# Performance work log

Measured on AMD Instinct MI355X. Metric: run time of the kernel, lower is better.

## Reference

```python
import math
import jax, jax.numpy as jnp
import numpy as np

# ---- config (from ModelConfig) ----
HIDDEN = 2880
HEAD_DIM = 64
N_HEADS = 64
N_KV = 8
Q_MULT = N_HEADS // N_KV  # 8
SLIDING_WINDOW = 128      # left context; causal windowed attention
ROPE_BASE = 150000.0
ROPE_SCALE = 32.0
NTK_ALPHA = 1.0
NTK_BETA = 32.0
INIT_CTX = 4096
RMS_EPS = 1e-5
SM_SCALE = 1.0 / math.sqrt(HEAD_DIM)
Q_DIM = N_HEADS * HEAD_DIM   # 4096
KV_DIM = N_KV * HEAD_DIM     # 512
QKV_DIM = Q_DIM + 2 * KV_DIM # 5120
B, T = 1, 2048


def _rope_cos_sin(n_tokens):
    """YaRN-scaled rotary cache, per RotaryEmbedding._compute_concentration_and_inv_freq."""
    d_half = HEAD_DIM // 2
    freq = ROPE_BASE ** (jnp.arange(0, HEAD_DIM, 2, dtype=jnp.float32) / HEAD_DIM)
    concentration = 0.1 * math.log(ROPE_SCALE) + 1.0
    low = d_half * math.log(INIT_CTX / (NTK_BETA * 2 * math.pi)) / math.log(ROPE_BASE)
    high = d_half * math.log(INIT_CTX / (NTK_ALPHA * 2 * math.pi)) / math.log(ROPE_BASE)
    interpolation = 1.0 / (ROPE_SCALE * freq)
    extrapolation = 1.0 / freq
    ramp = (jnp.arange(d_half, dtype=jnp.float32) - low) / (high - low)
    mask = 1.0 - jnp.clip(ramp, 0.0, 1.0)
    inv_freq = interpolation * (1.0 - mask) + extrapolation * mask
    pos = jnp.arange(n_tokens, dtype=jnp.float32)
    angles = pos[:, None] * inv_freq[None, :]  # [t, d/2]
    return jnp.cos(angles) * concentration, jnp.sin(angles) * concentration


def _apply_rope(x, cos, sin):
    """Interleaved RoPE (matches _apply_rotary_emb). x: [b, t, ..., d]."""
    shape = x.shape
    n_mid = x.ndim - 3  # dims between token axis and feature axis
    c = cos.reshape((1, shape[1]) + (1,) * n_mid + (shape[-1] // 2,))
    s = sin.reshape((1, shape[1]) + (1,) * n_mid + (shape[-1] // 2,))
    x1 = x[..., ::2]
    x2 = x[..., 1::2]
    o1 = x1 * c - x2 * s
    o2 = x2 * c + x1 * s
    return jnp.stack((o1, o2), axis=-1).reshape(shape)


def _rmsnorm(x, scale):
    t = x.astype(jnp.float32)
    t = t * jax.lax.rsqrt(jnp.mean(t * t, axis=-1, keepdims=True) + RMS_EPS)
    return (t * scale).astype(x.dtype)


def setup_inputs() -> dict:
    key = jax.random.key(0)
    ks = jax.random.split(key, 7)
    x = jax.random.normal(ks[0], (B, T, HIDDEN), dtype=jnp.float32)
    norm_scale = jnp.ones((HIDDEN,), dtype=jnp.float32)
    w_qkv = jax.random.normal(ks[1], (QKV_DIM, HIDDEN), dtype=jnp.float32) * (HIDDEN ** -0.5)
    b_qkv = jax.random.normal(ks[2], (QKV_DIM,), dtype=jnp.float32) * 0.02
    sinks = jax.random.normal(ks[3], (N_HEADS,), dtype=jnp.float32)
    w_out = jax.random.normal(ks[4], (HIDDEN, Q_DIM), dtype=jnp.float32) * (Q_DIM ** -0.5)
    b_out = jax.random.normal(ks[5], (HIDDEN,), dtype=jnp.float32) * 0.02
    return {"x": x, "norm_scale": norm_scale, "w_qkv": w_qkv, "b_qkv": b_qkv,
            "sinks": sinks, "w_out": w_out, "b_out": b_out}


def reference(x, norm_scale, w_qkv, b_qkv, sinks, w_out, b_out):
    b, t, _ = x.shape
    h = _rmsnorm(x, norm_scale)
    qkv = h @ w_qkv.T + b_qkv  # [b, t, 5120]
    q = qkv[..., :Q_DIM].reshape(b, t, N_KV, Q_MULT, HEAD_DIM)
    k = qkv[..., Q_DIM:Q_DIM + KV_DIM].reshape(b, t, N_KV, HEAD_DIM)
    v = qkv[..., Q_DIM + KV_DIM:].reshape(b, t, N_KV, HEAD_DIM)

    cos, sin = _rope_cos_sin(t)
    q = _apply_rope(q, cos, sin)
    k = _apply_rope(k, cos, sin)

    # sliding-window causal attention with sink logits (sdpa windowed path)
    left_ctx = SLIDING_WINDOW
    window = left_ctx + 1
    kp = jnp.pad(k, ((0, 0), (left_ctx, 0), (0, 0), (0, 0)))
    vp = jnp.pad(v, ((0, 0), (left_ctx, 0), (0, 0), (0, 0)))
    gather_idx = jnp.arange(t)[:, None] + jnp.arange(window)[None, :]  # into padded axis
    kwin = kp[:, gather_idx]  # [b, t, w, n_kv, d]
    vwin = vp[:, gather_idx]

    pos = jnp.arange(t)[:, None] + (jnp.arange(window) - left_ctx)[None, :]
    valid = (pos >= 0) & (pos < t)  # [t, w]

    scores = jnp.einsum('bthqd,btwhd->bthqw', q, kwin).astype(jnp.float32) * SM_SCALE
    scores = jnp.where(valid[None, :, None, None, :], scores, -jnp.inf)

    sink = (sinks * math.log(2.0)).reshape(N_KV, Q_MULT)
    sink = jnp.broadcast_to(sink[None, None, :, :, None], (b, t, N_KV, Q_MULT, 1))
    scores = jnp.concatenate([scores, sink], axis=-1)  # [b, t, h, q, w+1]

    w_attn = jax.nn.softmax(scores, axis=-1)[..., :-1].astype(v.dtype)
    attn = jnp.einsum('bthqw,btwhd->bthqd', w_attn, vwin).reshape(b, t, -1)

    out = attn @ w_out.T + b_out
    return x + out
```

## Files before the change

kernel.cpp:

```cpp
#include <hip/hip_runtime.h>
#include <math.h>

typedef unsigned short u16;
typedef unsigned int   u32;
using f32x4  = __attribute__((ext_vector_type(4))) float;
using bf16x8 = __attribute__((ext_vector_type(8))) __bf16;

#define HIDDEN   2880
#define QKVD     5120
#define QD       4096
#define TTOK     2048
#define NKV      8
#define QMULT    8
#define HD       64
#define NPAD     2944

#define PREP_QKV_BLOCKS  14400
#define PREP_WOUT_BLOCKS 11776
#define PREP_RMS_BLOCKS  2048

static __device__ __forceinline__ float bflo(u32 u){ return __uint_as_float(u << 16); }
static __device__ __forceinline__ float bfhi(u32 u){ return __uint_as_float(u & 0xffff0000u); }
static __device__ __forceinline__ u16 f2bf(float f){
    u32 u = __float_as_uint(f);
    u32 r = (u + 0x7fffu + ((u >> 16) & 1u)) >> 16;
    return (u16)r;
}

static __device__ __forceinline__ void glds16(const void* g, void* l) {
    __builtin_amdgcn_global_load_lds(
        (__attribute__((address_space(1))) void*)g,
        (__attribute__((address_space(3))) void*)l,
        16, 0, 0);
}

__global__ __launch_bounds__(256) void prep_kernel(const float* __restrict__ w_qkv,
                                                   u16* __restrict__ wqkv_bf,
                                                   const float* __restrict__ w_out,
                                                   u16* __restrict__ wout_bf,
                                                   const float* __restrict__ x,
                                                   const float* __restrict__ scale,
                                                   u16* __restrict__ h) {
    const int b = blockIdx.x;
    const int tid = threadIdx.x;
    if (b < PREP_QKV_BLOCKS) {
        int i = b * 256 + tid;
        float4 f = ((const float4*)w_qkv)[i];
        ushort4 o;
        o.x = f2bf(f.x); o.y = f2bf(f.y); o.z = f2bf(f.z); o.w = f2bf(f.w);
        ((ushort4*)wqkv_bf)[i] = o;
    } else if (b < PREP_QKV_BLOCKS + PREP_WOUT_BLOCKS) {
        int i = (b - PREP_QKV_BLOCKS) * 256 + tid;
        int idx = i * 4;
        int row = idx >> 12;
        int col = idx & 4095;
        ushort4 o;
        if (row < HIDDEN) {
            float4 f = *(const float4*)(w_out + (long)row * QD + col);
            o.x = f2bf(f.x); o.y = f2bf(f.y); o.z = f2bf(f.z); o.w = f2bf(f.w);
        } else {
            o.x = 0; o.y = 0; o.z = 0; o.w = 0;
        }
        ((ushort4*)wout_bf)[i] = o;
    } else {
        const int t = b - (PREP_QKV_BLOCKS + PREP_WOUT_BLOCKS);
        const float4* xr = (const float4*)(x + (long)t * HIDDEN);
        float4 v[3];
        float ss = 0.f;
        #pragma unroll
        for (int it = 0; it < 3; ++it) {
            int i4 = tid + it * 256;
            if (i4 < 720) {
                v[it] = xr[i4];
                ss += v[it].x*v[it].x + v[it].y*v[it].y + v[it].z*v[it].z + v[it].w*v[it].w;
            }
        }
        #pragma unroll
        for (int off = 32; off > 0; off >>= 1) ss += __shfl_down(ss, off);
        __shared__ float red[4];
        if ((tid & 63) == 0) red[tid >> 6] = ss;
        __syncthreads();
        float tot = red[0] + red[1] + red[2] + red[3];
        float rr = rsqrtf(tot * (1.0f / HIDDEN) + 1e-5f);
        ushort4* hr = (ushort4*)(h + (long)t * HIDDEN);
        #pragma unroll
        for (int it = 0; it < 3; ++it) {
            int i4 = tid + it * 256;
            if (i4 < 720) {
                float4 s4 = ((const float4*)scale)[i4];
                ushort4 o;
                o.x = f2bf(v[it].x * rr * s4.x);
                o.y = f2bf(v[it].y * rr * s4.y);
                o.z = f2bf(v[it].z * rr * s4.z);
                o.w = f2bf(v[it].w * rr * s4.w);
                hr[i4] = o;
            }
        }
    }
}

__global__ __launch_bounds__(256) void gemm_bt_part(const u16* __restrict__ A,
                                                    const u16* __restrict__ B,
                                                    u16* __restrict__ C0,
                                                    int N, int K, int ksplit) {
    __shared__ u16 lsA[2][128 * 32];
    __shared__ u16 lsB[2][128 * 32];
    const int tid  = threadIdx.x;
    const int lane = tid & 63;
    const int wv   = tid >> 6;
    const int wm   = wv >> 1, wn = wv & 1;
    const long m0 = (long)blockIdx.y * 128;
    const long n0 = (long)blockIdx.x * 128;
    const int kb = blockIdx.z * ksplit;
    const int ke = kb + ksplit;
    u16* C = C0 + (size_t)blockIdx.z * ((size_t)TTOK * N);

    f32x4 acc[4][4];
    #pragma unroll
    for (int i = 0; i < 4; ++i)
        #pragma unroll
        for (int j = 0; j < 4; ++j) acc[i][j] = f32x4{0.f, 0.f, 0.f, 0.f};

    const int sr = lane >> 2;
    const int sc = lane & 3;
    const int fr = lane & 15;
    const int fk = (lane >> 4) * 8;

    const u16* Abase = A + (m0 + wv * 32 + sr) * (long)K + sc * 8;
    const u16* Bbase = B + (n0 + wv * 32 + sr) * (long)K + sc * 8;
    const int ldsW = (wv * 32) * 32;
    const long rowK16 = 16 * (long)K;

    auto stage = [&](int k0, int buf) {
        glds16(Abase + k0,          &lsA[buf][ldsW]);
        glds16(Abase + k0 + rowK16, &lsA[buf][ldsW + 512]);
        glds16(Bbase + k0,          &lsB[buf][ldsW]);
        glds16(Bbase + k0 + rowK16, &lsB[buf][ldsW + 512]);
    };

    stage(kb, 0);
    int ib = 0;
    for (int k0 = kb; k0 < ke; k0 += 32, ib ^= 1) {
        __syncthreads();
        if (k0 + 32 < ke) stage(k0 + 32, ib ^ 1);
        bf16x8 af[4], bfg[4];
        #pragma unroll
        for (int mi = 0; mi < 4; ++mi)
            af[mi] = *(const bf16x8*)&lsA[ib][(wm * 64 + mi * 16 + fr) * 32 + fk];
        #pragma unroll
        for (int ni = 0; ni < 4; ++ni)
            bfg[ni] = *(const bf16x8*)&lsB[ib][(wn * 64 + ni * 16 + fr) * 32 + fk];
        #pragma unroll
        for (int mi = 0; mi < 4; ++mi)
            #pragma unroll
            for (int ni = 0; ni < 4; ++ni)
                acc[mi][ni] = __builtin_amdgcn_mfma_f32_16x16x32_bf16(af[mi], bfg[ni], acc[mi][ni], 0, 0, 0);
    }

    const int cr = (lane >> 4) * 4;
    const int cc = lane & 15;
    #pragma unroll
    for (int ni = 0; ni < 4; ++ni) {
        long col = n0 + wn * 64 + ni * 16 + cc;
        #pragma unroll
        for (int mi = 0; mi < 4; ++mi) {
            #pragma unroll
            for (int r2 = 0; r2 < 4; ++r2) {
                long row = m0 + wm * 64 + mi * 16 + cr + r2;
                C[row * (long)N + col] = f2bf(acc[mi][ni][r2]);
            }
        }
    }
}

__global__ __launch_bounds__(256) void rope_kernel(const u16* __restrict__ p1a,
                                                   const u16* __restrict__ p1b,
                                                   const float* __restrict__ b_qkv,
                                                   u16* __restrict__ qr,
                                                   u16* __restrict__ kr,
                                                   u16* __restrict__ vr) {
    const int t = blockIdx.x;
    const int tid = threadIdx.x;
    __shared__ float cs[32], sn[32];
    if (tid < 32) {
        float fi = (float)tid;
        float freq   = exp2f(17.1946032f * (fi * (1.0f / 32.0f)));
        float interp = 1.0f / (32.0f * freq);
        float extra  = 1.0f / freq;
        float ramp   = (fi - 8.0927802f) * (1.0f / (17.3980220f - 8.0927802f));
        float rc     = fminf(fmaxf(ramp, 0.0f), 1.0f);
        float invf   = interp * rc + extra * (1.0f - rc);
        float ang    = (float)t * invf;
        cs[tid] = cosf(ang) * 1.3465736f;
        sn[tid] = sinf(ang) * 1.3465736f;
    }
    __syncthreads();
    const u16* rowA = p1a + (long)t * QKVD;
    const u16* rowB = p1b + (long)t * QKVD;
    auto pair = [&](int col) -> float2 {
        u32 ua = *(const u32*)(rowA + col);
        u32 ub = *(const u32*)(rowB + col);
        float2 bb = *(const float2*)(b_qkv + col);
        return make_float2(bflo(ua) + bflo(ub) + bb.x, bfhi(ua) + bfhi(ub) + bb.y);
    };
    for (int p = tid; p < 2048; p += 256) {
        int hd2 = p >> 5, i = p & 31;
        float2 ab = pair(hd2 * 64 + 2 * i);
        float o1 = ab.x * cs[i] - ab.y * sn[i];
        float o2 = ab.y * cs[i] + ab.x * sn[i];
        *(u32*)(qr + (long)t * QD + hd2 * 64 + 2 * i) = (u32)f2bf(o1) | ((u32)f2bf(o2) << 16);
    }
    {
        int kv = tid >> 5, i = tid & 31;
        float2 ab = pair(QD + kv * 64 + 2 * i);
        float o1 = ab.x * cs[i] - ab.y * sn[i];
        float o2 = ab.y * cs[i] + ab.x * sn[i];
        *(u32*)(kr + ((long)kv * TTOK + t) * HD + 2 * i) = (u32)f2bf(o1) | ((u32)f2bf(o2) << 16);
    }
    {
        int kv = tid >> 5, d2 = tid & 31;
        float2 ab = pair(QD + 512 + kv * 64 + 2 * d2);
        *(u32*)(vr + ((long)kv * TTOK + t) * HD + 2 * d2) = (u32)f2bf(ab.x) | ((u32)f2bf(ab.y) << 16);
    }
}

__global__ __launch_bounds__(256, 2) void attn_kernel(const u16* __restrict__ qr,
                                                      const u16* __restrict__ kr,
                                                      const u16* __restrict__ vr,
                                                      const float* __restrict__ sinks,
                                                      u16* __restrict__ o) {
    const int t0  = blockIdx.x * 16;
    const int h   = blockIdx.y;
    const int qhg = blockIdx.z;
    const int tid = threadIdx.x;
    const int lane = tid & 63, wv = tid >> 6;
    __shared__ __align__(16) u16 ks[144][72];
    __shared__ __align__(16) u16 Vt[64][168];
    __shared__ __align__(16) u16 P [4][16][168];
    const u16* kb = kr + (long)h * TTOK * HD;
    const u16* vb = vr + (long)h * TTOK * HD;

    #pragma unroll
    for (int i = 0; i < 5; ++i) {
        int idx = i * 256 + tid;
        if (idx < 144 * 8) {
            int rr = idx >> 3, c = idx & 7;
            int tk = t0 - 128 + rr;
            int tks = tk < 0 ? 0 : tk;
            *(uint4*)&ks[rr][c * 8] = *(const uint4*)(kb + (long)tks * HD + c * 8);
        }
    }
    #pragma unroll
    for (int c4 = 0; c4 < 8; ++c4) {
        if (tid < 144) {
            int tk = t0 - 128 + tid;
            int tks = tk < 0 ? 0 : tk;
            uint4 v4 = *(const uint4*)(vb + (long)tks * HD + c4 * 8);
            int d0 = c4 * 8;
            Vt[d0+0][tid] = (u16)(v4.x & 0xffff); Vt[d0+1][tid] = (u16)(v4.x >> 16);
            Vt[d0+2][tid] = (u16)(v4.y & 0xffff); Vt[d0+3][tid] = (u16)(v4.y >> 16);
            Vt[d0+4][tid] = (u16)(v4.z & 0xffff); Vt[d0+5][tid] = (u16)(v4.z >> 16);
            Vt[d0+6][tid] = (u16)(v4.w & 0xffff); Vt[d0+7][tid] = (u16)(v4.w >> 16);
        }
    }
    if (tid < 128) {
        *(uint4*)&Vt[tid >> 1][144 + (tid & 1) * 8] = uint4{0, 0, 0, 0};
    }
    if (lane < 32) {
        *(uint4*)&P[wv][lane >> 1][144 + (lane & 1) * 8] = uint4{0, 0, 0, 0};
    }
    __syncthreads();

    const int qh   = qhg * 4 + wv;
    const int head = h * QMULT + qh;
    const int fr = lane & 15, fk = (lane >> 4) * 8;
    const int cr = (lane >> 4) * 4;

    const u16* qrow = qr + (long)(t0 + fr) * QD + head * HD;
    bf16x8 qf0 = *(const bf16x8*)(qrow + fk);
    bf16x8 qf1 = *(const bf16x8*)(qrow + 32 + fk);

    const int kmin = 128 - t0;
    float lsum[4] = {0.f, 0.f, 0.f, 0.f};

    for (int nt = 0; nt < 9; ++nt) {
        bf16x8 b0 = *(const bf16x8*)&ks[nt * 16 + fr][fk];
        bf16x8 b1 = *(const bf16x8*)&ks[nt * 16 + fr][32 + fk];
        f32x4 s = f32x4{0.f, 0.f, 0.f, 0.f};
        s = __builtin_amdgcn_mfma_f32_16x16x32_bf16(qf0, b0, s, 0, 0, 0);
        s = __builtin_amdgcn_mfma_f32_16x16x32_bf16(qf1, b1, s, 0, 0, 0);
        const int kk = nt * 16 + fr;
        #pragma unroll
        for (int r = 0; r < 4; ++r) {
            int row = cr + r;
            bool valid = (kk >= row) && (kk <= row + 128) && (kk >= kmin);
            float p = valid ? __expf(s[r] * 0.125f) : 0.0f;
            lsum[r] += p;
            P[wv][row][kk] = f2bf(p);
        }
    }

    f32x4 oacc[4];
    #pragma unroll
    for (int dt = 0; dt < 4; ++dt) oacc[dt] = f32x4{0.f, 0.f, 0.f, 0.f};
    #pragma unroll
    for (int k5 = 0; k5 < 5; ++k5) {
        const int k0 = k5 * 32;
        bf16x8 pa = *(const bf16x8*)&P[wv][fr][k0 + fk];
        #pragma unroll
        for (int dt = 0; dt < 4; ++dt) {
            bf16x8 vf = *(const bf16x8*)&Vt[dt * 16 + fr][k0 + fk];
            oacc[dt] = __builtin_amdgcn_mfma_f32_16x16x32_bf16(pa, vf, oacc[dt], 0, 0, 0);
        }
    }

    #pragma unroll
    for (int r = 0; r < 4; ++r) {
        float v = lsum[r];
        v += __shfl_xor(v, 1);
        v += __shfl_xor(v, 2);
        v += __shfl_xor(v, 4);
        v += __shfl_xor(v, 8);
        lsum[r] = v;
    }
    const float sk = exp2f(sinks[head]);
    float inv[4];
    #pragma unroll
    for (int r = 0; r < 4; ++r) inv[r] = 1.0f / (lsum[r] + sk);

    #pragma unroll
    for (int dt = 0; dt < 4; ++dt) {
        #pragma unroll
        for (int r = 0; r < 4; ++r) {
            o[(long)(t0 + cr + r) * QD + head * HD + dt * 16 + fr] = f2bf(oacc[dt][r] * inv[r]);
        }
    }
}

__global__ __launch_bounds__(256) void reduce2_kernel(const u16* __restrict__ p2a,
                                                      const u16* __restrict__ p2b,
                                                      const float* __restrict__ x,
                                                      const float* __restrict__ b_out,
                                                      float* __restrict__ out) {
    const int row = blockIdx.y;
    const int c4 = blockIdx.x * 256 + threadIdx.x;
    if (c4 >= 720) return;
    const int col = c4 * 4;
    ushort4 ua = *(const ushort4*)(p2a + (long)row * NPAD + col);
    ushort4 ub = *(const ushort4*)(p2b + (long)row * NPAD + col);
    float4 xv = *(const float4*)(x + (long)row * HIDDEN + col);
    float4 bv = *(const float4*)(b_out + col);
    float4 o;
    o.x = xv.x + bv.x + __uint_as_float((u32)ua.x << 16) + __uint_as_float((u32)ub.x << 16);
    o.y = xv.y + bv.y + __uint_as_float((u32)ua.y << 16) + __uint_as_float((u32)ub.y << 16);
    o.z = xv.z + bv.z + __uint_as_float((u32)ua.z << 16) + __uint_as_float((u32)ub.z << 16);
    o.w = xv.w + bv.w + __uint_as_float((u32)ua.w << 16) + __uint_as_float((u32)ub.w << 16);
    *(float4*)(out + (long)row * HIDDEN + col) = o;
}

extern "C" void kernel_launch(void* const* d_in, const int* in_sizes, int n_in,
                              void* d_out, int out_size, void* d_ws, size_t ws_size,
                              hipStream_t stream) {
    const float* x      = (const float*)d_in[0];
    const float* nscale = (const float*)d_in[1];
    const float* w_qkv  = (const float*)d_in[2];
    const float* b_qkv  = (const float*)d_in[3];
    const float* sinks  = (const float*)d_in[4];
    const float* w_out  = (const float*)d_in[5];
    const float* b_out  = (const float*)d_in[6];
    float* out = (float*)d_out;

    char* ws = (char*)d_ws;
    size_t off = 0;
    auto alloc = [&](size_t bytes) { void* p = ws + off; off += (bytes + 255) & ~(size_t)255; return p; };
    u16* wqkv_bf = (u16*)alloc((size_t)QKVD * HIDDEN * 2);
    u16* wout_bf = (u16*)alloc((size_t)NPAD * QD * 2);
    u16* h       = (u16*)alloc((size_t)TTOK * HIDDEN * 2);
    u16* p1      = (u16*)alloc((size_t)2 * TTOK * QKVD * 2);
    u16* qrot    = (u16*)alloc((size_t)TTOK * QD * 2);
    u16* krot    = (u16*)alloc((size_t)NKV * TTOK * HD * 2);
    u16* vrot    = (u16*)alloc((size_t)NKV * TTOK * HD * 2);
    u16* attn = wqkv_bf;
    u16* p2   = p1;

    prep_kernel<<<PREP_QKV_BLOCKS + PREP_WOUT_BLOCKS + PREP_RMS_BLOCKS, 256, 0, stream>>>(
        w_qkv, wqkv_bf, w_out, wout_bf, x, nscale, h);
    gemm_bt_part<<<dim3(QKVD / 128, TTOK / 128, 2), 256, 0, stream>>>(
        h, wqkv_bf, p1, QKVD, HIDDEN, HIDDEN / 2);
    rope_kernel<<<TTOK, 256, 0, stream>>>(
        p1, p1 + (size_t)TTOK * QKVD, b_qkv, qrot, krot, vrot);
    attn_kernel<<<dim3(TTOK / 16, NKV, 2), 256, 0, stream>>>(qrot, krot, vrot, sinks, attn);
    gemm_bt_part<<<dim3(NPAD / 128, TTOK / 128, 2), 256, 0, stream>>>(
        attn, wout_bf, p2, NPAD, QD, QD / 2);
    reduce2_kernel<<<dim3(3, TTOK), 256, 0, stream>>>(
        p2, p2 + (size_t)TTOK * NPAD, x, b_out, out);
}
```

Baseline: 359.4 us.

## Replace split-K GEMM with 256x256 eight-phase pipelined MFMA kernel

```diff
diff --git a/kernel.cpp b/kernel.cpp
--- a/kernel.cpp
+++ b/kernel.cpp
@@ -33,6 +33,8 @@
         (__attribute__((address_space(3))) void*)l,
         16, 0, 0);
 }
+
+#define BAR() asm volatile("s_barrier" ::: "memory")
 
 __global__ __launch_bounds__(256) void prep_kernel(const float* __restrict__ w_qkv,
                                                    u16* __restrict__ wqkv_bf,
@@ -99,62 +101,116 @@
     }
 }
 
-__global__ __launch_bounds__(256) void gemm_bt_part(const u16* __restrict__ A,
-                                                    const u16* __restrict__ B,
-                                                    u16* __restrict__ C0,
-                                                    int N, int K, int ksplit) {
-    __shared__ u16 lsA[2][128 * 32];
-    __shared__ u16 lsB[2][128 * 32];
+
+#define LOAD_AQ(MH) do { \
+    aq[0][0] = *(const bf16x8*)(aS + (2*(MH)+0)*2048 + off0); \
+    aq[0][1] = *(const bf16x8*)(aS + (2*(MH)+0)*2048 + off1); \
+    aq[1][0] = *(const bf16x8*)(aS + (2*(MH)+1)*2048 + off0); \
+    aq[1][1] = *(const bf16x8*)(aS + (2*(MH)+1)*2048 + off1); \
+} while (0)
+
+#define MFMA_Q(MH) do { \
+    __builtin_amdgcn_s_setprio(1); \
+    _Pragma("unroll") \
+    for (int i2_ = 0; i2_ < 2; ++i2_) { \
+        _Pragma("unroll") \
+        for (int ni_ = 0; ni_ < 4; ++ni_) { \
+            acc[2*(MH)+i2_][ni_] = __builtin_amdgcn_mfma_f32_16x16x32_bf16(aq[i2_][0], bq[ni_][0], acc[2*(MH)+i2_][ni_], 0, 0, 0); \
+            acc[2*(MH)+i2_][ni_] = __builtin_amdgcn_mfma_f32_16x16x32_bf16(aq[i2_][1], bq[ni_][1], acc[2*(MH)+i2_][ni_], 0, 0, 0); \
+        } \
+    } \
+    __builtin_amdgcn_s_setprio(0); \
+} while (0)
+
+__global__ __launch_bounds__(512, 2) void gemm_bt_8ph(const u16* __restrict__ A,
+                                                      const u16* __restrict__ B,
+                                                      u16* __restrict__ C0,
+                                                      int N, int K, int ksplit,
+                                                      int blimit, int colmax) {
+    extern __shared__ u16 smem[];
+    u16* const smA = smem;
+    u16* const smB = smem + 2 * 256 * 64;
     const int tid  = threadIdx.x;
     const int lane = tid & 63;
     const int wv   = tid >> 6;
-    const int wm   = wv >> 1, wn = wv & 1;
-    const long m0 = (long)blockIdx.y * 128;
-    const long n0 = (long)blockIdx.x * 128;
-    const int kb = blockIdx.z * ksplit;
-    const int ke = kb + ksplit;
+    const int wm   = wv >> 2;
+    const int wn   = wv & 3;
+    const long m0  = (long)blockIdx.y * 256;
+    const long n0  = (long)blockIdx.x * 256;
+    const int kbase = blockIdx.z * ksplit;
+    const int NT   = ksplit >> 6;
     u16* C = C0 + (size_t)blockIdx.z * ((size_t)TTOK * N);
 
-    f32x4 acc[4][4];
-    #pragma unroll
-    for (int i = 0; i < 4; ++i)
+    const int srow = tid >> 3;
+    const int sg8  = ((tid & 7) ^ (srow & 7)) << 3;
+    const int fr   = lane & 15;
+    const int off0 = ((lane >> 4) << 4) ^ ((lane & 7) << 4);
+    const int off1 = off0 ^ 64;
+    const char* aR = (const char*)smA + (wm * 128 + fr) * 128;
+    const char* bR = (const char*)smB + (wn * 64  + fr) * 128;
+
+    f32x4 acc[8][4];
+    #pragma unroll
+    for (int i = 0; i < 8; ++i)
         #pragma unroll
         for (int j = 0; j < 4; ++j) acc[i][j] = f32x4{0.f, 0.f, 0.f, 0.f};
 
-    const int sr = lane >> 2;
-    const int sc = lane & 3;
-    const int fr = lane & 15;
-    const int fk = (lane >> 4) * 8;
-
-    const u16* Abase = A + (m0 + wv * 32 + sr) * (long)K + sc * 8;
-    const u16* Bbase = B + (n0 + wv * 32 + sr) * (long)K + sc * 8;
-    const int ldsW = (wv * 32) * 32;
-    const long rowK16 = 16 * (long)K;
-
-    auto stage = [&](int k0, int buf) {
-        glds16(Abase + k0,          &lsA[buf][ldsW]);
-        glds16(Abase + k0 + rowK16, &lsA[buf][ldsW + 512]);
-        glds16(Bbase + k0,          &lsB[buf][ldsW]);
-        glds16(Bbase + k0 + rowK16, &lsB[buf][ldsW + 512]);
+    const u16* Asrc = A + (m0 + srow) * (long)K + kbase + sg8;
+    auto stageA = [&](int t) {
+        char* dst = (char*)smA + (t & 1) * 32768 + (wv * 8) * 128;
+        const u16* src = Asrc + t * 64;
+        #pragma unroll
+        for (int hj = 0; hj < 4; ++hj)
+            glds16(src + (size_t)(hj * 64) * K, dst + hj * 64 * 128);
     };
-
-    stage(kb, 0);
-    int ib = 0;
-    for (int k0 = kb; k0 < ke; k0 += 32, ib ^= 1) {
-        __syncthreads();
-        if (k0 + 32 < ke) stage(k0 + 32, ib ^ 1);
-        bf16x8 af[4], bfg[4];
-        #pragma unroll
-        for (int mi = 0; mi < 4; ++mi)
-            af[mi] = *(const bf16x8*)&lsA[ib][(wm * 64 + mi * 16 + fr) * 32 + fk];
-        #pragma unroll
-        for (int ni = 0; ni < 4; ++ni)
-            bfg[ni] = *(const bf16x8*)&lsB[ib][(wn * 64 + ni * 16 + fr) * 32 + fk];
-        #pragma unroll
-        for (int mi = 0; mi < 4; ++mi)
-            #pragma unroll
-            for (int ni = 0; ni < 4; ++ni)
-                acc[mi][ni] = __builtin_amdgcn_mfma_f32_16x16x32_bf16(af[mi], bfg[ni], acc[mi][ni], 0, 0, 0);
+    auto stageB = [&](int t, int h) {
+        char* dst = (char*)smB + (t & 1) * 32768 + (h * 128 + wv * 8) * 128;
+        #pragma unroll
+        for (int j = 0; j < 2; ++j) {
+            long r = n0 + h * 128 + j * 64 + srow;
+            if (r > blimit) r = blimit;
+            glds16(B + (size_t)r * K + kbase + t * 64 + sg8, dst + j * 64 * 128);
+        }
+    };
+
+    stageA(0);
+    stageB(0, 0); stageB(0, 1);
+    if (NT > 1) { stageB(1, 0); stageB(1, 1); }
+    if (NT < 3) asm volatile("s_waitcnt vmcnt(0)" ::: "memory");
+    else        asm volatile("s_waitcnt vmcnt(4)" ::: "memory");
+    BAR();
+
+    for (int t = 0; t < NT; ++t) {
+        const int sof = (t & 1) * 32768;
+        const char* aS = aR + sof;
+        const char* bS = bR + sof;
+        bf16x8 bq[4][2], aq[2][2];
+        #pragma unroll
+        for (int ni = 0; ni < 4; ++ni) {
+            bq[ni][0] = *(const bf16x8*)(bS + ni * 2048 + off0);
+            bq[ni][1] = *(const bf16x8*)(bS + ni * 2048 + off1);
+        }
+        LOAD_AQ(0);
+        if (t + 1 < NT) stageA(t + 1);
+        BAR();
+        MFMA_Q(0);
+        BAR();
+        LOAD_AQ(1);
+        if (t + 2 < NT) stageB(t + 2, 0);
+        BAR();
+        MFMA_Q(1);
+        BAR();
+        LOAD_AQ(2);
+        if (t + 2 < NT) stageB(t + 2, 1);
+        BAR();
+        MFMA_Q(2);
+        BAR();
+        LOAD_AQ(3);
+        BAR();
+        MFMA_Q(3);
+        if (t >= NT - 2) asm volatile("s_waitcnt vmcnt(0)" ::: "memory");
+        else             asm volatile("s_waitcnt vmcnt(4)" ::: "memory");
+        BAR();
     }
 
     const int cr = (lane >> 4) * 4;
@@ -162,19 +218,19 @@
     #pragma unroll
     for (int ni = 0; ni < 4; ++ni) {
         long col = n0 + wn * 64 + ni * 16 + cc;
-        #pragma unroll
-        for (int mi = 0; mi < 4; ++mi) {
+        if (col < colmax) {
             #pragma unroll
-            for (int r2 = 0; r2 < 4; ++r2) {
-                long row = m0 + wm * 64 + mi * 16 + cr + r2;
-                C[row * (long)N + col] = f2bf(acc[mi][ni][r2]);
+            for (int mi = 0; mi < 8; ++mi) {
+                long row = m0 + wm * 128 + mi * 16 + cr;
+                #pragma unroll
+                for (int r2 = 0; r2 < 4; ++r2)
+                    C[(row + r2) * (long)N + col] = f2bf(acc[mi][ni][r2]);
             }
         }
     }
 }
 
-__global__ __launch_bounds__(256) void rope_kernel(const u16* __restrict__ p1a,
-                                                   const u16* __restrict__ p1b,
+__global__ __launch_bounds__(256) void rope_kernel(const u16* __restrict__ p1,
                                                    const float* __restrict__ b_qkv,
                                                    u16* __restrict__ qr,
                                                    u16* __restrict__ kr,
@@ -195,13 +251,11 @@
         sn[tid] = sinf(ang) * 1.3465736f;
     }
     __syncthreads();
-    const u16* rowA = p1a + (long)t * QKVD;
-    const u16* rowB = p1b + (long)t * QKVD;
+    const u16* rowA = p1 + (long)t * QKVD;
     auto pair = [&](int col) -> float2 {
         u32 ua = *(const u32*)(rowA + col);
-        u32 ub = *(const u32*)(rowB + col);
         float2 bb = *(const float2*)(b_qkv + col);
-        return make_float2(bflo(ua) + bflo(ub) + bb.x, bfhi(ua) + bfhi(ub) + bb.y);
+        return make_float2(bflo(ua) + bb.x, bfhi(ua) + bb.y);
     };
     for (int p = tid; p < 2048; p += 256) {
         int hd2 = p >> 5, i = p & 31;
@@ -370,6 +424,13 @@
     const float* b_out  = (const float*)d_in[6];
     float* out = (float*)d_out;
 
+    static int smem_set = 0;
+    if (!smem_set) {
+        hipFuncSetAttribute((const void*)gemm_bt_8ph,
+                            hipFuncAttributeMaxDynamicSharedMemorySize, 131072);
+        smem_set = 1;
+    }
+
     char* ws = (char*)d_ws;
     size_t off = 0;
     auto alloc = [&](size_t bytes) { void* p = ws + off; off += (bytes + 255) & ~(size_t)255; return p; };
@@ -385,13 +446,12 @@
 
     prep_kernel<<<PREP_QKV_BLOCKS + PREP_WOUT_BLOCKS + PREP_RMS_BLOCKS, 256, 0, stream>>>(
         w_qkv, wqkv_bf, w_out, wout_bf, x, nscale, h);
-    gemm_bt_part<<<dim3(QKVD / 128, TTOK / 128, 2), 256, 0, stream>>>(
-        h, wqkv_bf, p1, QKVD, HIDDEN, HIDDEN / 2);
-    rope_kernel<<<TTOK, 256, 0, stream>>>(
-        p1, p1 + (size_t)TTOK * QKVD, b_qkv, qrot, krot, vrot);
+    gemm_bt_8ph<<<dim3(QKVD / 256, TTOK / 256, 1), 512, 131072, stream>>>(
+        h, wqkv_bf, p1, QKVD, HIDDEN, HIDDEN, QKVD - 1, QKVD);
+    rope_kernel<<<TTOK, 256, 0, stream>>>(p1, b_qkv, qrot, krot, vrot);
     attn_kernel<<<dim3(TTOK / 16, NKV, 2), 256, 0, stream>>>(qrot, krot, vrot, sinks, attn);
-    gemm_bt_part<<<dim3(NPAD / 128, TTOK / 128, 2), 256, 0, stream>>>(
-        attn, wout_bf, p2, NPAD, QD, QD / 2);
+    gemm_bt_8ph<<<dim3((NPAD + 255) / 256, TTOK / 256, 2), 512, 131072, stream>>>(
+        attn, wout_bf, p2, NPAD, QD, QD / 2, NPAD - 1, NPAD);
     reduce2_kernel<<<dim3(3, TTOK), 256, 0, stream>>>(
         p2, p2 + (size_t)TTOK * NPAD, x, b_out, out);
 }
```

Result: faster. 345.3 us (-3.9%).
